# Kernel optimization log

Measured on AMD Instinct MI355X. Metric: run time of the kernel, lower is better.

The kernel has to match this reference:

```python
import jax, jax.numpy as jnp
import numpy as np

# Fixed hyperparameters from init_kwargs
KH, KW = 3, 3
GRID_SIZE = 5
SPLINE_ORDER = 3
GRID_RANGE = (-1.0, 1.0)


def _make_grid():
    # grid buffer: arange(-k, grid_size + k + 1) * h + grid_range[0], shape (G + 2k + 1,) = (12,)
    h = (GRID_RANGE[1] - GRID_RANGE[0]) / GRID_SIZE
    return (jnp.arange(-SPLINE_ORDER, GRID_SIZE + SPLINE_ORDER + 1, dtype=jnp.float32) * h
            + GRID_RANGE[0])


def _unfold(x):
    # torch.nn.Unfold with kernel (3,3), stride 1, pad 0, dilation 1.
    # Returns (N, C*KH*KW) with channel-major ordering (c, i, j), matching torch.
    B, C, H, W = x.shape
    Ho, Wo = H - KH + 1, W - KW + 1
    cols = [x[:, :, i:i + Ho, j:j + Wo] for i in range(KH) for j in range(KW)]
    p = jnp.stack(cols, axis=2)                    # (B, C, KH*KW, Ho, Wo)
    p = p.reshape(B, C * KH * KW, Ho * Wo)         # (B, in_features, L)
    p = p.transpose(0, 2, 1).reshape(-1, C * KH * KW)  # (B*L, in_features)
    return p, Ho, Wo


def _b_splines(x, grid):
    # x: (N, in_features); grid: (G + 2k + 1,) uniform, shared across features.
    # Returns (N, in_features, G + k) B-spline basis via Cox-de Boor recursion.
    x = x[..., None]  # (N, in, 1)
    bases = ((x >= grid[:-1]) & (x < grid[1:])).astype(x.dtype)  # (N, in, G+2k)
    for k in range(1, SPLINE_ORDER + 1):
        left = (x - grid[: -(k + 1)]) / (grid[k:-1] - grid[: -(k + 1)])
        right = (grid[k + 1:] - x) / (grid[k + 1:] - grid[1:-k])
        bases = left * bases[..., :-1] + right * bases[..., 1:]
    return bases  # (N, in, G + k)


def setup_inputs() -> dict:
    key = jax.random.key(0)
    k1, k2, k3, k4 = jax.random.split(key, 4)
    in_features = 32 * KH * KW  # 288
    out_features = 64
    n_coef = GRID_SIZE + SPLINE_ORDER  # 8
    x = jax.random.normal(k1, (16, 32, 64, 64), dtype=jnp.float32)
    base_weight = jax.random.normal(k2, (out_features, in_features), dtype=jnp.float32) * (1.0 / np.sqrt(in_features))
    spline_weight = jax.random.normal(k3, (out_features, in_features, n_coef), dtype=jnp.float32) * 0.1
    spline_scaler = jax.random.normal(k4, (out_features, in_features), dtype=jnp.float32) * (1.0 / np.sqrt(in_features))
    return {"x": x, "base_weight": base_weight, "spline_weight": spline_weight,
            "spline_scaler": spline_scaler}


def reference(x, base_weight, spline_weight, spline_scaler):
    B = x.shape[0]
    out_features = base_weight.shape[0]
    grid = _make_grid()

    patches, Ho, Wo = _unfold(x)                              # (N, in_features)
    N, in_features = patches.shape

    # KANLinear forward
    base_out = jnp.matmul(jax.nn.relu(patches), base_weight.T)  # (N, out)
    bases = _b_splines(patches, grid)                           # (N, in, G+k)
    scaled_w = spline_weight * spline_scaler[..., None]         # (out, in, G+k)
    spline_out = jnp.matmul(bases.reshape(N, -1), scaled_w.reshape(out_features, -1).T)
    out = base_out + spline_out                                 # (N, out)

    out = out.reshape(B, Ho, Wo, out_features).transpose(0, 3, 1, 2)  # (B, C_out, Ho, Wo)
    return out
```

## Files before the change

### kernel.cpp

```cpp
#include <hip/hip_runtime.h>
#include <stdint.h>

typedef _Float16 half8  __attribute__((ext_vector_type(8)));
typedef float    f32x16 __attribute__((ext_vector_type(16)));
typedef uint32_t u32x4  __attribute__((ext_vector_type(4)));

#define NPIX 61504
#define LPB  3844
#define NOUT 64
#define NXPIX 2097152
#define WTAB_HALF8 20736
#define BFRAG_BYTES 332800
#define WS_NEED ((size_t)BFRAG_BYTES + (size_t)NXPIX * 16)


__global__ void prep_w(const float* __restrict__ bw,
                       const float* __restrict__ sw,
                       const float* __restrict__ sc,
                       half8* __restrict__ wt) {
  int t = blockIdx.x * 256 + threadIdx.x;
  half8 v;
  int fi, h, o;
  if (t < 64 * 288) {
    o = t / 288;
    int f = t - o * 288;
    float scale = sc[t];
    const float* p = sw + t * 8;
#pragma unroll
    for (int j = 0; j < 8; ++j) v[j] = (_Float16)(p[j] * scale);
    int c  = (f * 57) >> 9;
    int r  = f - c * 9;
    int i2 = (r * 11) >> 5;
    int j2 = r - i2 * 3;
    int st = (i2 * 3 + j2) * 16 + (c >> 1);
    h  = c & 1;
    fi = st * 2 + (o >> 5);
  } else {
    int t2 = t - 64 * 288;
    o = t2 / 36;
    int g8 = t2 - o * 36;
    const float* p = bw + o * 288 + g8 * 8;
#pragma unroll
    for (int j = 0; j < 8; ++j) v[j] = (_Float16)p[j];
    int stb = g8 >> 1;
    h  = g8 & 1;
    fi = (144 + stb) * 2 + (o >> 5);
  }
  wt[fi * 64 + h * 32 + (o & 31)] = v;
}

__device__ inline half8 bspline8(float xv) {
  float u = fmaf(xv, 2.5f, 5.5f);
  float fi = floorf(u);
  int i = (int)fi;
  float t = u - fi, s = 1.0f - t;
  float t2 = t * t, t3 = t2 * t;
  float s2 = s * s, s3 = s2 * s;
  float w3 = t3 * 0.16666667f;
  float w0 = s3 * 0.16666667f;
  float w1 = fmaf(0.5f, t3, -t2) + 0.66666667f;
  float w2 = fmaf(0.5f, s3, -s2) + 0.66666667f;
  uint32_t u01 = __builtin_bit_cast(uint32_t, __builtin_amdgcn_cvt_pkrtz(w0, w1));
  uint32_t u23 = __builtin_bit_cast(uint32_t, __builtin_amdgcn_cvt_pkrtz(w2, w3));
  uint64_t V = (uint64_t)u01 | ((uint64_t)u23 << 32);
  uint32_t vl = (uint32_t)(V << 16);
  u32x4 fr;
#pragma unroll
  for (int q = 0; q < 4; ++q) {
    int d = i - 2 * q;
    uint32_t rr = (uint32_t)(V >> ((48 - 16 * d) & 63));
    fr[q] = ((uint32_t)d <= 3u) ? rr : ((d == 4) ? vl : 0u);
  }
  return __builtin_bit_cast(half8, fr);
}

__global__ void precompute_basis(const float* __restrict__ x,
                                 half8* __restrict__ bsp) {
  int i = blockIdx.x * 256 + threadIdx.x;
  bsp[i] = bspline8(x[i]);
}

__device__ inline void stage_chunk(const half8* __restrict__ s, half8* d,
                                   int nhalf8, int lane) {
  for (int it = 0; it < nhalf8; it += 64) {
#if __has_builtin(__builtin_amdgcn_global_load_lds)
    __builtin_amdgcn_global_load_lds(
        (const __attribute__((address_space(1))) uint32_t*)(s + it + lane),
        (__attribute__((address_space(3))) uint32_t*)(d + it),
        16, 0, 0);
#else
    d[it + lane] = s[it + lane];
#endif
  }
}

__global__ __launch_bounds__(128) void kan_main3(
    const float* __restrict__ x,
    const half8* __restrict__ bsp,
    const half8* __restrict__ wt,
    float* __restrict__ out) {
  __shared__ half8 smw[2][2048];

  const int tid  = threadIdx.x;
  const int lane = tid & 63;
  const int wv   = tid >> 6;
  const int l31  = lane & 31;
  const int h    = lane >> 5;

  int bid  = blockIdx.x;
  int tile = (bid < 480) ? ((bid & 7) * 60 + (bid >> 3)) : 480;
  const int pxw = tile * 128 + wv * 64;

  int xb[2];
#pragma unroll
  for (int np = 0; np < 2; ++np) {
    int p = pxw + np * 32 + l31;
    if (p > NPIX - 1) p = NPIX - 1;
    int b  = p / LPB;
    int l  = p - b * LPB;
    int ho = l / 62;
    int wo = l - ho * 62;
    xb[np] = b * 131072 + ho * 64 + wo;
  }

  f32x16 acc[2][2];
#pragma unroll
  for (int mo = 0; mo < 2; ++mo)
#pragma unroll
    for (int np = 0; np < 2; ++np)
#pragma unroll
      for (int i = 0; i < 16; ++i) acc[mo][np][i] = 0.f;

  stage_chunk(wt + 0, &smw[0][0] + wv * 1024 - wv * 1024 + wv * 1024, 0, 0);
  stage_chunk(wt + wv * 1024, &smw[0][wv * 1024], 1024, lane);

  int buf = 0;
  for (int ch = 0; ch < 11; ++ch) {
    __syncthreads();
    if (ch < 10) {
      int nfr  = (ch < 9) ? 2048 : 256;
      int half = ((ch + 1 < 10) ? 2048 : 256) >> 1;
      (void)nfr;
      stage_chunk(wt + (ch + 1) * 2048 + wv * half, &smw[buf ^ 1][wv * half],
                  half, lane);
    }
    const half8* wb = &smw[buf][0];

    if (ch < 9) {
      int i2 = (ch * 11) >> 5;
      int j2 = ch - i2 * 3;
      const half8* bp0 = bsp + xb[0] + h * 4096 + i2 * 64 + j2;
      const half8* bp1 = bsp + xb[1] + h * 4096 + i2 * 64 + j2;
#pragma unroll
      for (int stl = 0; stl < 16; ++stl) {
        half8 b0 = bp0[stl * 8192];
        half8 b1 = bp1[stl * 8192];
        half8 a0 = wb[stl * 128 + lane];
        half8 a1 = wb[stl * 128 + 64 + lane];
        acc[0][0] = __builtin_amdgcn_mfma_f32_32x32x16_f16(a0, b0, acc[0][0], 0, 0, 0);
        acc[0][1] = __builtin_amdgcn_mfma_f32_32x32x16_f16(a0, b1, acc[0][1], 0, 0, 0);
        acc[1][0] = __builtin_amdgcn_mfma_f32_32x32x16_f16(a1, b0, acc[1][0], 0, 0, 0);
        acc[1][1] = __builtin_amdgcn_mfma_f32_32x32x16_f16(a1, b1, acc[1][1], 0, 0, 0);
      }
    } else {
      int nst = (ch == 9) ? 16 : 2;
      for (int stl = 0; stl < nst; ++stl) {
        int stb = (ch - 9) * 16 + stl;
        int fb0 = stb * 16 + h * 8;
        half8 bb[2];
#pragma unroll
        for (int np = 0; np < 2; ++np) {
          u32x4 pk;
#pragma unroll
          for (int jj = 0; jj < 4; ++jj) {
            float v0, v1;
            {
              int f = fb0 + jj * 2;
              int c = (f * 57) >> 9; int r = f - c * 9;
              int a = (r * 11) >> 5; int b2 = r - a * 3;
              v0 = fmaxf(x[xb[np] + c * 4096 + a * 64 + b2], 0.f);
            }
            {
              int f = fb0 + jj * 2 + 1;
              int c = (f * 57) >> 9; int r = f - c * 9;
              int a = (r * 11) >> 5; int b2 = r - a * 3;
              v1 = fmaxf(x[xb[np] + c * 4096 + a * 64 + b2], 0.f);
            }
            pk[jj] = __builtin_bit_cast(uint32_t, __builtin_amdgcn_cvt_pkrtz(v0, v1));
          }
          bb[np] = __builtin_bit_cast(half8, pk);
        }
        half8 a0 = wb[stl * 128 + lane];
        half8 a1 = wb[stl * 128 + 64 + lane];
        acc[0][0] = __builtin_amdgcn_mfma_f32_32x32x16_f16(a0, bb[0], acc[0][0], 0, 0, 0);
        acc[0][1] = __builtin_amdgcn_mfma_f32_32x32x16_f16(a0, bb[1], acc[0][1], 0, 0, 0);
        acc[1][0] = __builtin_amdgcn_mfma_f32_32x32x16_f16(a1, bb[0], acc[1][0], 0, 0, 0);
        acc[1][1] = __builtin_amdgcn_mfma_f32_32x32x16_f16(a1, bb[1], acc[1][1], 0, 0, 0);
      }
    }
    buf ^= 1;
  }

#pragma unroll
  for (int np = 0; np < 2; ++np) {
    int p = pxw + np * 32 + l31;
    bool ok = p < NPIX;
    int pc = ok ? p : NPIX - 1;
    int b = pc / LPB;
    int l = pc - b * LPB;
    float* ob = out + b * (NOUT * LPB) + l;
#pragma unroll
    for (int mo = 0; mo < 2; ++mo)
#pragma unroll
      for (int rg = 0; rg < 16; ++rg) {
        int o = mo * 32 + (rg & 3) + 8 * (rg >> 2) + 4 * h;
        if (ok) ob[o * LPB] = acc[mo][np][rg];
      }
  }
}

extern "C" void kernel_launch(void* const* d_in, const int* in_sizes, int n_in,
                              void* d_out, int out_size, void* d_ws, size_t ws_size,
                              hipStream_t stream) {
  const float* x  = (const float*)d_in[0];
  const float* bw = (const float*)d_in[1];
  const float* sw = (const float*)d_in[2];
  const float* sc = (const float*)d_in[3];
  float* out = (float*)d_out;
  half8* wt  = (half8*)d_ws;
  half8* bsp = (half8*)((char*)d_ws + BFRAG_BYTES);

  prep_w<<<81, 256, 0, stream>>>(bw, sw, sc, wt);
  precompute_basis<<<NXPIX / 256, 256, 0, stream>>>(x, bsp);
  kan_main3<<<481, 128, 0, stream>>>(x, bsp, wt, out);
}
```

Measured before the change: 145.3 us.

## Merge prep kernels and software-pipeline basis loads with register prefetch

Folds the weight-prep and basis-precompute kernels into one launch, which removes a kernel boundary. In the main kernel, basis fragments are prefetched PF=4 steps ahead into registers, and the prefetch carries over into the next chunk, so global load latency overlaps with MFMA work. The base (ReLU) chunk becomes a single 18-step pass staged in one larger LDS buffer, and the kernel adds a launch-bounds occupancy hint of 2 blocks. The cost is more register pressure from the prefetch buffers and a larger shared-memory footprint.

```diff
diff --git a/kernel.cpp b/kernel.cpp
--- a/kernel.cpp
+++ b/kernel.cpp
@@ -9,45 +9,9 @@
 #define LPB  3844
 #define NOUT 64
 #define NXPIX 2097152
-#define WTAB_HALF8 20736
 #define BFRAG_BYTES 332800
-#define WS_NEED ((size_t)BFRAG_BYTES + (size_t)NXPIX * 16)
-
-
-__global__ void prep_w(const float* __restrict__ bw,
-                       const float* __restrict__ sw,
-                       const float* __restrict__ sc,
-                       half8* __restrict__ wt) {
-  int t = blockIdx.x * 256 + threadIdx.x;
-  half8 v;
-  int fi, h, o;
-  if (t < 64 * 288) {
-    o = t / 288;
-    int f = t - o * 288;
-    float scale = sc[t];
-    const float* p = sw + t * 8;
-#pragma unroll
-    for (int j = 0; j < 8; ++j) v[j] = (_Float16)(p[j] * scale);
-    int c  = (f * 57) >> 9;
-    int r  = f - c * 9;
-    int i2 = (r * 11) >> 5;
-    int j2 = r - i2 * 3;
-    int st = (i2 * 3 + j2) * 16 + (c >> 1);
-    h  = c & 1;
-    fi = st * 2 + (o >> 5);
-  } else {
-    int t2 = t - 64 * 288;
-    o = t2 / 36;
-    int g8 = t2 - o * 36;
-    const float* p = bw + o * 288 + g8 * 8;
-#pragma unroll
-    for (int j = 0; j < 8; ++j) v[j] = (_Float16)p[j];
-    int stb = g8 >> 1;
-    h  = g8 & 1;
-    fi = (144 + stb) * 2 + (o >> 5);
-  }
-  wt[fi * 64 + h * 32 + (o & 31)] = v;
-}
+#define PF 4
+
 
 __device__ inline half8 bspline8(float xv) {
   float u = fmaf(xv, 2.5f, 5.5f);
@@ -74,32 +38,71 @@
   return __builtin_bit_cast(half8, fr);
 }
 
-__global__ void precompute_basis(const float* __restrict__ x,
-                                 half8* __restrict__ bsp) {
-  int i = blockIdx.x * 256 + threadIdx.x;
-  bsp[i] = bspline8(x[i]);
-}
-
-__device__ inline void stage_chunk(const half8* __restrict__ s, half8* d,
-                                   int nhalf8, int lane) {
-  for (int it = 0; it < nhalf8; it += 64) {
+__global__ void prep_all(const float* __restrict__ x,
+                         const float* __restrict__ bw,
+                         const float* __restrict__ sw,
+                         const float* __restrict__ sc,
+                         half8* __restrict__ bsp,
+                         half8* __restrict__ wt) {
+  int bid = blockIdx.x;
+  if (bid < 8192) {
+    int i = bid * 256 + threadIdx.x;
+    bsp[i] = bspline8(x[i]);
+    return;
+  }
+  int t = (bid - 8192) * 256 + threadIdx.x;
+  half8 v;
+  int fi, h, o;
+  if (t < 64 * 288) {
+    o = t / 288;
+    int f = t - o * 288;
+    float scale = sc[t];
+    const float* p = sw + t * 8;
+#pragma unroll
+    for (int j = 0; j < 8; ++j) v[j] = (_Float16)(p[j] * scale);
+    int c  = (f * 57) >> 9;
+    int r  = f - c * 9;
+    int i2 = (r * 11) >> 5;
+    int j2 = r - i2 * 3;
+    int st = (i2 * 3 + j2) * 16 + (c >> 1);
+    h  = c & 1;
+    fi = st * 2 + (o >> 5);
+  } else {
+    int t2 = t - 64 * 288;
+    o = t2 / 36;
+    int g8 = t2 - o * 36;
+    const float* p = bw + o * 288 + g8 * 8;
+#pragma unroll
+    for (int j = 0; j < 8; ++j) v[j] = (_Float16)p[j];
+    int stb = g8 >> 1;
+    h  = g8 & 1;
+    fi = (144 + stb) * 2 + (o >> 5);
+  }
+  wt[fi * 64 + h * 32 + (o & 31)] = v;
+}
+
+__device__ inline void stage(const half8* __restrict__ s, half8* d,
+                             int n128, int tid) {
+  int wv = tid >> 6, lane = tid & 63;
+  for (int it = 0; it < n128; ++it) {
+    int off = it * 128 + wv * 64;
 #if __has_builtin(__builtin_amdgcn_global_load_lds)
     __builtin_amdgcn_global_load_lds(
-        (const __attribute__((address_space(1))) uint32_t*)(s + it + lane),
-        (__attribute__((address_space(3))) uint32_t*)(d + it),
+        (const __attribute__((address_space(1))) uint32_t*)(s + off + lane),
+        (__attribute__((address_space(3))) uint32_t*)(d + off),
         16, 0, 0);
 #else
-    d[it + lane] = s[it + lane];
+    d[off + lane] = s[off + lane];
 #endif
   }
 }
 
-__global__ __launch_bounds__(128) void kan_main3(
+__global__ __launch_bounds__(128, 2) void kan_main4(
     const float* __restrict__ x,
     const half8* __restrict__ bsp,
     const half8* __restrict__ wt,
     float* __restrict__ out) {
-  __shared__ half8 smw[2][2048];
+  __shared__ half8 smw[2][2304];
 
   const int tid  = threadIdx.x;
   const int lane = tid & 63;
@@ -131,74 +134,88 @@
 #pragma unroll
       for (int i = 0; i < 16; ++i) acc[mo][np][i] = 0.f;
 
-  stage_chunk(wt + 0, &smw[0][0] + wv * 1024 - wv * 1024 + wv * 1024, 0, 0);
-  stage_chunk(wt + wv * 1024, &smw[0][wv * 1024], 1024, lane);
+  stage(wt, &smw[0][0], 16, tid);
+
+  const half8* pb0 = bsp + xb[0] + h * 4096;
+  const half8* pb1 = bsp + xb[1] + h * 4096;
+  half8 b0r[PF], b1r[PF];
+#pragma unroll
+  for (int p = 0; p < PF; ++p) {
+    b0r[p] = pb0[p * 8192];
+    b1r[p] = pb1[p * 8192];
+  }
 
   int buf = 0;
-  for (int ch = 0; ch < 11; ++ch) {
+  for (int ch = 0; ch < 9; ++ch) {
     __syncthreads();
-    if (ch < 10) {
-      int nfr  = (ch < 9) ? 2048 : 256;
-      int half = ((ch + 1 < 10) ? 2048 : 256) >> 1;
-      (void)nfr;
-      stage_chunk(wt + (ch + 1) * 2048 + wv * half, &smw[buf ^ 1][wv * half],
-                  half, lane);
+    if (ch < 8) stage(wt + (ch + 1) * 2048, &smw[buf ^ 1][0], 16, tid);
+    else        stage(wt + 18432,           &smw[buf ^ 1][0], 18, tid);
+
+    int i2n = ((ch + 1) * 11) >> 5;
+    int j2n = (ch + 1) - i2n * 3;
+    const half8* nb0 = bsp + xb[0] + h * 4096 + i2n * 64 + j2n;
+    const half8* nb1 = bsp + xb[1] + h * 4096 + i2n * 64 + j2n;
+    const half8* wb = &smw[buf][0];
+
+#pragma unroll
+    for (int stl = 0; stl < 16; ++stl) {
+      const int slot = stl & (PF - 1);
+      half8 b0 = b0r[slot], b1 = b1r[slot];
+      if (stl + PF < 16) {
+        b0r[slot] = pb0[(stl + PF) * 8192];
+        b1r[slot] = pb1[(stl + PF) * 8192];
+      } else {
+        b0r[slot] = nb0[(stl + PF - 16) * 8192];
+        b1r[slot] = nb1[(stl + PF - 16) * 8192];
+      }
+      half8 a0 = wb[stl * 128 + lane];
+      half8 a1 = wb[stl * 128 + 64 + lane];
+      acc[0][0] = __builtin_amdgcn_mfma_f32_32x32x16_f16(a0, b0, acc[0][0], 0, 0, 0);
+      acc[0][1] = __builtin_amdgcn_mfma_f32_32x32x16_f16(a0, b1, acc[0][1], 0, 0, 0);
+      acc[1][0] = __builtin_amdgcn_mfma_f32_32x32x16_f16(a1, b0, acc[1][0], 0, 0, 0);
+      acc[1][1] = __builtin_amdgcn_mfma_f32_32x32x16_f16(a1, b1, acc[1][1], 0, 0, 0);
     }
+    pb0 = nb0;
+    pb1 = nb1;
+    buf ^= 1;
+  }
+
+  __syncthreads();
+  {
     const half8* wb = &smw[buf][0];
-
-    if (ch < 9) {
-      int i2 = (ch * 11) >> 5;
-      int j2 = ch - i2 * 3;
-      const half8* bp0 = bsp + xb[0] + h * 4096 + i2 * 64 + j2;
-      const half8* bp1 = bsp + xb[1] + h * 4096 + i2 * 64 + j2;
-#pragma unroll
-      for (int stl = 0; stl < 16; ++stl) {
-        half8 b0 = bp0[stl * 8192];
-        half8 b1 = bp1[stl * 8192];
-        half8 a0 = wb[stl * 128 + lane];
-        half8 a1 = wb[stl * 128 + 64 + lane];
-        acc[0][0] = __builtin_amdgcn_mfma_f32_32x32x16_f16(a0, b0, acc[0][0], 0, 0, 0);
-        acc[0][1] = __builtin_amdgcn_mfma_f32_32x32x16_f16(a0, b1, acc[0][1], 0, 0, 0);
-        acc[1][0] = __builtin_amdgcn_mfma_f32_32x32x16_f16(a1, b0, acc[1][0], 0, 0, 0);
-        acc[1][1] = __builtin_amdgcn_mfma_f32_32x32x16_f16(a1, b1, acc[1][1], 0, 0, 0);
+#pragma unroll
+    for (int stb = 0; stb < 18; ++stb) {
+      int fb0 = stb * 16 + h * 8;
+      half8 bb[2];
+#pragma unroll
+      for (int np = 0; np < 2; ++np) {
+        u32x4 pk;
+#pragma unroll
+        for (int jj = 0; jj < 4; ++jj) {
+          float v0, v1;
+          {
+            int f = fb0 + jj * 2;
+            int c = (f * 57) >> 9; int r = f - c * 9;
+            int a = (r * 11) >> 5; int b2 = r - a * 3;
+            v0 = fmaxf(x[xb[np] + c * 4096 + a * 64 + b2], 0.f);
+          }
+          {
+            int f = fb0 + jj * 2 + 1;
+            int c = (f * 57) >> 9; int r = f - c * 9;
+            int a = (r * 11) >> 5; int b2 = r - a * 3;
+            v1 = fmaxf(x[xb[np] + c * 4096 + a * 64 + b2], 0.f);
+          }
+          pk[jj] = __builtin_bit_cast(uint32_t, __builtin_amdgcn_cvt_pkrtz(v0, v1));
+        }
+        bb[np] = __builtin_bit_cast(half8, pk);
       }
-    } else {
-      int nst = (ch == 9) ? 16 : 2;
-      for (int stl = 0; stl < nst; ++stl) {
-        int stb = (ch - 9) * 16 + stl;
-        int fb0 = stb * 16 + h * 8;
-        half8 bb[2];
-#pragma unroll
-        for (int np = 0; np < 2; ++np) {
-          u32x4 pk;
-#pragma unroll
-          for (int jj = 0; jj < 4; ++jj) {
-            float v0, v1;
-            {
-              int f = fb0 + jj * 2;
-              int c = (f * 57) >> 9; int r = f - c * 9;
-              int a = (r * 11) >> 5; int b2 = r - a * 3;
-              v0 = fmaxf(x[xb[np] + c * 4096 + a * 64 + b2], 0.f);
-            }
-            {
-              int f = fb0 + jj * 2 + 1;
-              int c = (f * 57) >> 9; int r = f - c * 9;
-              int a = (r * 11) >> 5; int b2 = r - a * 3;
-              v1 = fmaxf(x[xb[np] + c * 4096 + a * 64 + b2], 0.f);
-            }
-            pk[jj] = __builtin_bit_cast(uint32_t, __builtin_amdgcn_cvt_pkrtz(v0, v1));
-          }
-          bb[np] = __builtin_bit_cast(half8, pk);
-        }
-        half8 a0 = wb[stl * 128 + lane];
-        half8 a1 = wb[stl * 128 + 64 + lane];
-        acc[0][0] = __builtin_amdgcn_mfma_f32_32x32x16_f16(a0, bb[0], acc[0][0], 0, 0, 0);
-        acc[0][1] = __builtin_amdgcn_mfma_f32_32x32x16_f16(a0, bb[1], acc[0][1], 0, 0, 0);
-        acc[1][0] = __builtin_amdgcn_mfma_f32_32x32x16_f16(a1, bb[0], acc[1][0], 0, 0, 0);
-        acc[1][1] = __builtin_amdgcn_mfma_f32_32x32x16_f16(a1, bb[1], acc[1][1], 0, 0, 0);
-      }
+      half8 a0 = wb[stb * 128 + lane];
+      half8 a1 = wb[stb * 128 + 64 + lane];
+      acc[0][0] = __builtin_amdgcn_mfma_f32_32x32x16_f16(a0, bb[0], acc[0][0], 0, 0, 0);
+      acc[0][1] = __builtin_amdgcn_mfma_f32_32x32x16_f16(a0, bb[1], acc[0][1], 0, 0, 0);
+      acc[1][0] = __builtin_amdgcn_mfma_f32_32x32x16_f16(a1, bb[0], acc[1][0], 0, 0, 0);
+      acc[1][1] = __builtin_amdgcn_mfma_f32_32x32x16_f16(a1, bb[1], acc[1][1], 0, 0, 0);
     }
-    buf ^= 1;
   }
 
 #pragma unroll
@@ -230,7 +247,6 @@
   half8* wt  = (half8*)d_ws;
   half8* bsp = (half8*)((char*)d_ws + BFRAG_BYTES);
 
-  prep_w<<<81, 256, 0, stream>>>(bw, sw, sc, wt);
-  precompute_basis<<<NXPIX / 256, 256, 0, stream>>>(x, bsp);
-  kan_main3<<<481, 128, 0, stream>>>(x, bsp, wt, out);
-}
+  prep_all<<<8192 + 81, 256, 0, stream>>>(x, bw, sw, sc, bsp, wt);
+  kan_main4<<<481, 128, 0, stream>>>(x, bsp, wt, out);
+}
```

Measured after the change: 132.9 us. 8.5% less time.
